# Kernel tuning notes

Measured on AMD Instinct MI355X. Metric: run time of the kernel, lower is better.

Reference implementation:

```python
import jax, jax.numpy as jnp
import numpy as np

B, S, I, H = 256, 50, 1024, 512
SENT, DOC = 512, 1024
SEGMENTS, MAXPOS = 4, 25
POS_SZ, SEG_SZ = 50, 50


def _gru_dir(xg, W_hh, b_hh):
    # xg: [S,B,3H] precomputed input gates; returns hidden states [S,B,H]
    Hh = W_hh.shape[1]

    def step(h, xg_t):
        hg = h @ W_hh.T + b_hh  # [B,3H]
        r = jax.nn.sigmoid(xg_t[:, :Hh] + hg[:, :Hh])
        z = jax.nn.sigmoid(xg_t[:, Hh:2 * Hh] + hg[:, Hh:2 * Hh])
        n = jnp.tanh(xg_t[:, 2 * Hh:] + r * hg[:, 2 * Hh:])
        h = (1.0 - z) * n + z * h
        return h, h

    h0 = jnp.zeros((xg.shape[1], Hh), xg.dtype)
    _, hs = jax.lax.scan(step, h0, xg)
    return hs


def setup_inputs() -> dict:
    key = jax.random.key(0)
    ks = jax.random.split(key, 24)
    sc = 0.05
    inp = {
        'x': jax.random.normal(ks[0], (B, S, I), jnp.float32),
        'num_sentences': jnp.full((B,), S, jnp.int32),
        # GRU forward direction
        'W_ih_f': jax.random.normal(ks[1], (3 * H, I), jnp.float32) * sc,
        'W_hh_f': jax.random.normal(ks[2], (3 * H, H), jnp.float32) * sc,
        'b_ih_f': jax.random.normal(ks[3], (3 * H,), jnp.float32) * sc,
        'b_hh_f': jax.random.normal(ks[4], (3 * H,), jnp.float32) * sc,
        # GRU backward direction
        'W_ih_b': jax.random.normal(ks[5], (3 * H, I), jnp.float32) * sc,
        'W_hh_b': jax.random.normal(ks[6], (3 * H, H), jnp.float32) * sc,
        'b_ih_b': jax.random.normal(ks[7], (3 * H,), jnp.float32) * sc,
        'b_hh_b': jax.random.normal(ks[8], (3 * H,), jnp.float32) * sc,
        # sentence_rep: Linear(2H -> SENT) + ReLU
        'W_sent': jax.random.normal(ks[9], (SENT, 2 * H), jnp.float32) * sc,
        'b_sent': jax.random.normal(ks[10], (SENT,), jnp.float32) * sc,
        # content_logits: Linear(SENT -> 1)
        'w_content': jax.random.normal(ks[11], (SENT,), jnp.float32) * sc,
        'b_content': jax.random.normal(ks[12], (1,), jnp.float32) * sc,
        # document_rep: Linear(SENT->DOC), tanh, Linear(DOC->SENT)
        'W_d1': jax.random.normal(ks[13], (DOC, SENT), jnp.float32) * sc,
        'b_d1': jax.random.normal(ks[14], (DOC,), jnp.float32) * sc,
        'W_d2': jax.random.normal(ks[15], (SENT, DOC), jnp.float32) * sc,
        'b_d2': jax.random.normal(ks[16], (SENT,), jnp.float32) * sc,
        # Bilinear(SENT, SENT, 1, bias=False) weight
        'W_sim': jax.random.normal(ks[17], (SENT, SENT), jnp.float32) * sc,
        'bias': jnp.zeros((1,), jnp.float32),
        # position / segment encoders (embedding row 0 is padding -> zeros)
        'pos_emb': (jax.random.normal(ks[18], (MAXPOS + 1, POS_SZ), jnp.float32) * sc).at[0].set(0.0),
        'pos_lin': jax.random.normal(ks[19], (POS_SZ,), jnp.float32) * sc,
        'seg_emb': (jax.random.normal(ks[20], (SEGMENTS + 1, SEG_SZ), jnp.float32) * sc).at[0].set(0.0),
        'seg_lin': jax.random.normal(ks[21], (SEG_SZ,), jnp.float32) * sc,
    }
    return inp


def reference(x, num_sentences, W_ih_f, W_hh_f, b_ih_f, b_hh_f,
              W_ih_b, W_hh_b, b_ih_b, b_hh_b,
              W_sent, b_sent, w_content, b_content,
              W_d1, b_d1, W_d2, b_d2, W_sim, bias,
              pos_emb, pos_lin, seg_emb, seg_lin):
    xs = jnp.transpose(x, (1, 0, 2))  # [S,B,I] (time-major, uniform lengths)

    # Bidirectional GRU
    xg_f = jnp.einsum('sbi,gi->sbg', xs, W_ih_f) + b_ih_f
    hs_f = _gru_dir(xg_f, W_hh_f, b_hh_f)  # [S,B,H]
    xg_b = jnp.einsum('sbi,gi->sbg', xs[::-1], W_ih_b) + b_ih_b
    hs_b = _gru_dir(xg_b, W_hh_b, b_hh_b)[::-1]  # [S,B,H]
    rnn_out = jnp.concatenate([hs_f, hs_b], axis=-1)  # [S,B,2H]
    rnn_out = jnp.transpose(rnn_out, (1, 0, 2))  # [B,S,2H]

    # sentence representations
    sent = jax.nn.relu(jnp.einsum('bsh,dh->bsd', rnn_out, W_sent) + b_sent)  # [B,S,SENT]

    content = jnp.einsum('bsd,d->bs', sent, w_content) + b_content[0]

    avg = sent.sum(axis=1) / num_sentences[:, None].astype(sent.dtype)  # [B,SENT]
    doc = jnp.tanh(avg @ W_d1.T + b_d1) @ W_d2.T + b_d2  # [B,SENT]
    salience = jnp.einsum('bsd,bd->bs', sent, doc)

    # position / segment logits (faithful to original ordering: rel computed pre-clamp)
    abs_pos = jnp.arange(1, S + 1)[None, :].astype(jnp.float32)  # [1,S]
    chunk = jnp.round(num_sentences.astype(jnp.float32) / SEGMENTS)[:, None]  # [B,1]
    rel = jnp.clip(jnp.ceil(abs_pos / chunk), 0, SEGMENTS).astype(jnp.int32)  # [B,S]
    abs_idx = jnp.clip(jnp.arange(1, S + 1), 0, MAXPOS)  # [S]
    pos_logits = pos_emb[abs_idx] @ pos_lin  # [S]
    seg_logits = seg_emb[rel] @ seg_lin  # [B,S]

    static = content + salience + pos_logits[None, :] + seg_logits + bias[0]  # [B,S]

    # sequential novelty scan
    def step(summary, inputs):
        s_t, static_t = inputs  # [B,SENT], [B]
        sim = jnp.einsum('bi,ij,bj->b', s_t, W_sim, jnp.tanh(summary))
        logit = static_t - sim
        summary = summary + s_t * jax.nn.sigmoid(logit)[:, None]
        return summary, logit

    sent_tm = jnp.transpose(sent, (1, 0, 2))  # [S,B,SENT]
    summary0 = jnp.zeros((x.shape[0], SENT), sent.dtype)
    _, logits = jax.lax.scan(step, summary0, (sent_tm, static.T))  # [S,B]
    return logits[:, :, None]  # [S,B,1]
```

## Files before the change

kernel.cpp:

```cpp
#include <hip/hip_runtime.h>
#include <hip/hip_bf16.h>
#include <math.h>

#define B_    256
#define S_    50
#define I_    1024
#define H_    512
#define G3_   1536
#define SENT_ 512
#define DOC_  1024

typedef short bf16x8 __attribute__((ext_vector_type(8)));
typedef float f32x4 __attribute__((ext_vector_type(4)));

__device__ __forceinline__ float sigf(float x) { return 1.0f / (1.0f + __expf(-x)); }

__device__ __forceinline__ void gload16(const void* g, void* l) {
  __builtin_amdgcn_global_load_lds((const __attribute__((address_space(1))) void*)g,
                                   (__attribute__((address_space(3))) void*)l, 16, 0, 0);
}

__global__ __launch_bounds__(256) void mfma_xg(
    const __hip_bfloat16* __restrict__ x,
    const __hip_bfloat16* __restrict__ Wf, const float* __restrict__ bf_,
    const __hip_bfloat16* __restrict__ Wb, const float* __restrict__ bb_,
    __hip_bfloat16* __restrict__ xgf, __hip_bfloat16* __restrict__ xgb) {
  __shared__ __align__(16) short As[128 * 64];
  __shared__ __align__(16) short Ws[128 * 64];
  const int dir = blockIdx.z;
  const __hip_bfloat16* W = dir ? Wb : Wf;
  const float* bias = dir ? bb_ : bf_;
  __hip_bfloat16* out = dir ? xgb : xgf;
  const int tid = threadIdx.x;
  const int m0 = blockIdx.y * 128, n0 = blockIdx.x * 128;
  const int s = blockIdx.y >> 1, b_base = (blockIdx.y & 1) * 128;
  const int s_eff = dir ? (S_ - 1 - s) : s;
  const int lane = tid & 63, w = tid >> 6;
  const int moff = (w & 1) * 64, noff = (w >> 1) * 64;
  const int frow = lane & 15, quad = lane >> 4;
  const int rr = tid >> 3, gs = tid & 7;
  f32x4 acc[4][4] = {};
  for (int kc = 0; kc < I_; kc += 64) {
#pragma unroll
    for (int iss = 0; iss < 4; iss++) {
      int r = iss * 32 + rr;
      int col = kc + ((gs ^ (r & 7)) << 3);
      gload16(x + ((size_t)(b_base + r) * S_ + s_eff) * I_ + col, &As[(iss * 256 + w * 64) * 8]);
    }
#pragma unroll
    for (int iss = 0; iss < 4; iss++) {
      int r = iss * 32 + rr;
      int col = kc + ((gs ^ (r & 7)) << 3);
      gload16(W + (size_t)(n0 + r) * I_ + col, &Ws[(iss * 256 + w * 64) * 8]);
    }
    __syncthreads();
#pragma unroll
    for (int ks = 0; ks < 2; ks++) {
      int kg = ks * 4 + quad;
      bf16x8 af[4], bfr[4];
#pragma unroll
      for (int mf = 0; mf < 4; mf++) {
        int r = moff + mf * 16 + frow;
        af[mf] = *(const bf16x8*)&As[(r * 8 + (kg ^ (r & 7))) * 8];
      }
#pragma unroll
      for (int nf = 0; nf < 4; nf++) {
        int r = noff + nf * 16 + frow;
        bfr[nf] = *(const bf16x8*)&Ws[(r * 8 + (kg ^ (r & 7))) * 8];
      }
#pragma unroll
      for (int mf = 0; mf < 4; mf++)
#pragma unroll
        for (int nf = 0; nf < 4; nf++)
          acc[mf][nf] = __builtin_amdgcn_mfma_f32_16x16x32_bf16(af[mf], bfr[nf], acc[mf][nf], 0, 0, 0);
    }
    __syncthreads();
  }
#pragma unroll
  for (int mf = 0; mf < 4; mf++) {
    int rowb = m0 + moff + mf * 16 + quad * 4;
#pragma unroll
    for (int nf = 0; nf < 4; nf++) {
      int col = n0 + noff + nf * 16 + frow;
      float bv = bias[col];
      f32x4 c = acc[mf][nf];
#pragma unroll
      for (int rg = 0; rg < 4; rg++)
        out[(size_t)(rowb + rg) * G3_ + col] = __float2bfloat16(c[rg] + bv);
    }
  }
}

template <int ACT, bool HASBIAS>
__global__ __launch_bounds__(256) void mfma_nt(
    const __hip_bfloat16* __restrict__ A, const __hip_bfloat16* __restrict__ W,
    const float* __restrict__ bias, __hip_bfloat16* __restrict__ outb, int N, int K) {
  __shared__ __align__(16) short As[128 * 64];
  __shared__ __align__(16) short Ws[128 * 64];
  const int tid = threadIdx.x;
  const int m0 = blockIdx.y * 128, n0 = blockIdx.x * 128;
  const int lane = tid & 63, w = tid >> 6;
  const int moff = (w & 1) * 64, noff = (w >> 1) * 64;
  const int frow = lane & 15, quad = lane >> 4;
  const int rr = tid >> 3, gs = tid & 7;
  f32x4 acc[4][4] = {};
  for (int kc = 0; kc < K; kc += 64) {
#pragma unroll
    for (int iss = 0; iss < 4; iss++) {
      int r = iss * 32 + rr;
      int col = kc + ((gs ^ (r & 7)) << 3);
      gload16(A + (size_t)(m0 + r) * K + col, &As[(iss * 256 + w * 64) * 8]);
    }
#pragma unroll
    for (int iss = 0; iss < 4; iss++) {
      int r = iss * 32 + rr;
      int col = kc + ((gs ^ (r & 7)) << 3);
      gload16(W + (size_t)(n0 + r) * K + col, &Ws[(iss * 256 + w * 64) * 8]);
    }
    __syncthreads();
#pragma unroll
    for (int ks = 0; ks < 2; ks++) {
      int kg = ks * 4 + quad;
      bf16x8 af[4], bfr[4];
#pragma unroll
      for (int mf = 0; mf < 4; mf++) {
        int r = moff + mf * 16 + frow;
        af[mf] = *(const bf16x8*)&As[(r * 8 + (kg ^ (r & 7))) * 8];
      }
#pragma unroll
      for (int nf = 0; nf < 4; nf++) {
        int r = noff + nf * 16 + frow;
        bfr[nf] = *(const bf16x8*)&Ws[(r * 8 + (kg ^ (r & 7))) * 8];
      }
#pragma unroll
      for (int mf = 0; mf < 4; mf++)
#pragma unroll
        for (int nf = 0; nf < 4; nf++)
          acc[mf][nf] = __builtin_amdgcn_mfma_f32_16x16x32_bf16(af[mf], bfr[nf], acc[mf][nf], 0, 0, 0);
    }
    __syncthreads();
  }
#pragma unroll
  for (int mf = 0; mf < 4; mf++) {
    int rowb = m0 + moff + mf * 16 + quad * 4;
#pragma unroll
    for (int nf = 0; nf < 4; nf++) {
      int col = n0 + noff + nf * 16 + frow;
      float bv = HASBIAS ? bias[col] : 0.f;
      f32x4 c = acc[mf][nf];
#pragma unroll
      for (int rg = 0; rg < 4; rg++) {
        float v = c[rg] + bv;
        if (ACT == 1) v = fmaxf(v, 0.f);
        outb[(size_t)(rowb + rg) * N + col] = __float2bfloat16(v);
      }
    }
  }
}

__global__ __launch_bounds__(256, 1) void gru_persistent(
    const __hip_bfloat16* __restrict__ xgf, const __hip_bfloat16* __restrict__ xgb,
    const __hip_bfloat16* __restrict__ Wpf, const __hip_bfloat16* __restrict__ Wpb,
    const float* __restrict__ bhhf, const float* __restrict__ bhhb,
    __hip_bfloat16* __restrict__ h16a, __hip_bfloat16* __restrict__ h16b,
    __hip_bfloat16* __restrict__ rnn,
    unsigned int* __restrict__ arrive) {
  const int bid = blockIdx.x;
  const int dir = bid >> 7;
  const int bt = (bid >> 5) & 3;
  const int jt = bid & 31;
  const int g8 = bid >> 5;
  const int tid = threadIdx.x;
  const int w = tid >> 6, lane = tid & 63;
  const int frow = lane & 15, quad = lane >> 4;
  const __hip_bfloat16* xg = dir ? xgb : xgf;
  const __hip_bfloat16* Wp = dir ? Wpb : Wpf;
  const float* bhh = dir ? bhhb : bhhf;

  unsigned int* my_flag = arrive + bid * 64;

  const int j = jt * 16 + frow;
  const int brow0 = bt * 64 + w * 16 + quad * 4;
  const float br = bhh[j], bz = bhh[H_ + j], bn = bhh[2 * H_ + j];

  bf16x8 wf[3][16];
#pragma unroll
  for (int g = 0; g < 3; g++)
#pragma unroll
    for (int ks = 0; ks < 16; ks++)
      wf[g][ks] = *(const bf16x8*)(Wp + (size_t)(jt * 48 + g * 16 + frow) * H_ + ks * 32 + quad * 8);

  float hreg[4] = {0.f, 0.f, 0.f, 0.f};
  union U16 { unsigned long long q[2]; bf16x8 v; };

  for (int t = 0; t < S_; t++) {
    const __hip_bfloat16* hp = (t & 1) ? h16b : h16a;
    __hip_bfloat16* hn = (t & 1) ? h16a : h16b;
    float xgv[4][3];
#pragma unroll
    for (int rg = 0; rg < 4; rg++) {
      const __hip_bfloat16* xr = xg + ((size_t)t * B_ + brow0 + rg) * G3_;
      xgv[rg][0] = __bfloat162float(xr[j]);
      xgv[rg][1] = __bfloat162float(xr[H_ + j]);
      xgv[rg][2] = __bfloat162float(xr[2 * H_ + j]);
    }
    const __hip_bfloat16* hprow = hp + (size_t)(dir * B_ + bt * 64 + w * 16 + frow) * H_;
    bf16x8 af[16];
#pragma unroll
    for (int ks = 0; ks < 16; ks++) {
      const unsigned long long* p = (const unsigned long long*)(hprow + ks * 32 + quad * 8);
      U16 u;
      u.q[0] = __hip_atomic_load(p, __ATOMIC_RELAXED, __HIP_MEMORY_SCOPE_AGENT);
      u.q[1] = __hip_atomic_load(p + 1, __ATOMIC_RELAXED, __HIP_MEMORY_SCOPE_AGENT);
      af[ks] = u.v;
    }
    f32x4 acc[3] = {};
#pragma unroll
    for (int ks = 0; ks < 16; ks++)
#pragma unroll
      for (int g = 0; g < 3; g++)
        acc[g] = __builtin_amdgcn_mfma_f32_16x16x32_bf16(af[ks], wf[g][ks], acc[g], 0, 0, 0);

    const int s_orig = dir ? (S_ - 1 - t) : t;
#pragma unroll
    for (int rg = 0; rg < 4; rg++) {
      int b = brow0 + rg;
      float r = sigf(xgv[rg][0] + acc[0][rg] + br);
      float z = sigf(xgv[rg][1] + acc[1][rg] + bz);
      float n = tanhf(xgv[rg][2] + r * (acc[2][rg] + bn));
      float h = (1.f - z) * n + z * hreg[rg];
      hreg[rg] = h;
      __hip_bfloat16 hb = __float2bfloat16(h);
      unsigned short us;
      __builtin_memcpy(&us, &hb, 2);
      __hip_atomic_store((unsigned short*)(hn + (size_t)(dir * B_ + b) * H_ + j), us,
                         __ATOMIC_RELAXED, __HIP_MEMORY_SCOPE_AGENT);
      rnn[((size_t)b * S_ + s_orig) * (2 * H_) + dir * H_ + j] = hb;
    }

    if (t + 1 < S_) {
      __syncthreads();
      if (tid == 0)
        __hip_atomic_store(my_flag, (unsigned)(t + 1), __ATOMIC_RELAXED,
                           __HIP_MEMORY_SCOPE_AGENT);
      if (w == 0) {
        unsigned int* fl = arrive + ((size_t)(g8 * 32 + (lane & 31))) * 64;
        for (int spin = 0; spin < (1 << 17); spin++) {
          unsigned v = (lane < 32)
                           ? __hip_atomic_load(fl, __ATOMIC_RELAXED, __HIP_MEMORY_SCOPE_AGENT)
                           : (unsigned)(t + 1);
          if (__ballot(v >= (unsigned)(t + 1)) == ~0ull) break;
          __builtin_amdgcn_s_sleep(1);
        }
      }
      __syncthreads();
    }
  }
}

template <int ACT>
__global__ __launch_bounds__(256) void gemm_nt(const float* __restrict__ A,
                                               const float* __restrict__ W,
                                               const float* __restrict__ bias,
                                               float* __restrict__ C, int N, int K) {
  __shared__ float As[16][68];
  __shared__ float Bs[16][68];
  const int t = threadIdx.x;
  const int tx = t & 15, ty = t >> 4;
  const int m0 = blockIdx.y * 64, n0 = blockIdx.x * 64;
  const int lr = t >> 2, lc = t & 3;
  const float* Arow = A + (size_t)(m0 + lr) * K;
  const float* Wrow = W + (size_t)(n0 + lr) * K;
  float acc[4][4] = {};
  for (int kc = 0; kc < K; kc += 16) {
    float4 av = *(const float4*)(Arow + kc + lc * 4);
    float4 wv = *(const float4*)(Wrow + kc + lc * 4);
    As[lc * 4 + 0][lr] = av.x; As[lc * 4 + 1][lr] = av.y;
    As[lc * 4 + 2][lr] = av.z; As[lc * 4 + 3][lr] = av.w;
    Bs[lc * 4 + 0][lr] = wv.x; Bs[lc * 4 + 1][lr] = wv.y;
    Bs[lc * 4 + 2][lr] = wv.z; Bs[lc * 4 + 3][lr] = wv.w;
    __syncthreads();
#pragma unroll
    for (int k = 0; k < 16; k++) {
      float4 a4 = *(const float4*)&As[k][ty * 4];
      float4 b4 = *(const float4*)&Bs[k][tx * 4];
      float ar[4] = {a4.x, a4.y, a4.z, a4.w};
      float br[4] = {b4.x, b4.y, b4.z, b4.w};
#pragma unroll
      for (int i = 0; i < 4; i++)
#pragma unroll
        for (int jx = 0; jx < 4; jx++) acc[i][jx] = fmaf(ar[i], br[jx], acc[i][jx]);
    }
    __syncthreads();
  }
  float4 bv = *(const float4*)&bias[n0 + tx * 4];
  float bb[4] = {bv.x, bv.y, bv.z, bv.w};
#pragma unroll
  for (int i = 0; i < 4; i++) {
    float o[4];
#pragma unroll
    for (int jx = 0; jx < 4; jx++) {
      float v = acc[i][jx] + bb[jx];
      if (ACT == 1) v = fmaxf(v, 0.f);
      if (ACT == 2) v = tanhf(v);
      o[jx] = v;
    }
    *(float4*)&C[(size_t)(m0 + ty * 4 + i) * N + n0 + tx * 4] = float4{o[0], o[1], o[2], o[3]};
  }
}

__global__ void cast_kernel(const float* __restrict__ in, __hip_bfloat16* __restrict__ out, int n) {
  int i = (blockIdx.x * blockDim.x + threadIdx.x) * 4;
  if (i + 3 < n) {
    float4 v = *(const float4*)(in + i);
    out[i + 0] = __float2bfloat16(v.x);
    out[i + 1] = __float2bfloat16(v.y);
    out[i + 2] = __float2bfloat16(v.z);
    out[i + 3] = __float2bfloat16(v.w);
  }
}

__global__ void pack_whh(const float* __restrict__ Whh, __hip_bfloat16* __restrict__ outp) {
  int idx = blockIdx.x * 256 + threadIdx.x;
  if (idx >= G3_ * H_) return;
  int k = idx & 511;
  int row = idx >> 9;
  int g = row >> 9, j = row & 511;
  int p = (j >> 4) * 48 + g * 16 + (j & 15);
  outp[(size_t)p * H_ + k] = __float2bfloat16(Whh[idx]);
}

__global__ void tcast_wsim(const float* __restrict__ Wsim, __hip_bfloat16* __restrict__ outT) {
  int idx = blockIdx.x * 256 + threadIdx.x;
  if (idx >= SENT_ * SENT_) return;
  int i = idx >> 9, j = idx & 511;
  outT[(size_t)j * SENT_ + i] = __float2bfloat16(Wsim[idx]);
}

__global__ __launch_bounds__(256) void avg_kernel(const __hip_bfloat16* __restrict__ sent,
                                                  const int* __restrict__ ns,
                                                  float* __restrict__ avg) {
  int b = blockIdx.x, tid = threadIdx.x;
  const __hip_bfloat16* base = sent + (size_t)b * S_ * SENT_;
  float a0 = 0.f, a1 = 0.f;
  for (int s = 0; s < S_; s++) {
    a0 += __bfloat162float(base[s * SENT_ + tid]);
    a1 += __bfloat162float(base[s * SENT_ + 256 + tid]);
  }
  float inv = 1.0f / (float)ns[b];
  avg[(size_t)b * SENT_ + tid] = a0 * inv;
  avg[(size_t)b * SENT_ + 256 + tid] = a1 * inv;
}

__global__ void posseg_kernel(const float* __restrict__ pos_emb, const float* __restrict__ pos_lin,
                              const float* __restrict__ seg_emb, const float* __restrict__ seg_lin,
                              float* __restrict__ pos_logits, float* __restrict__ seg_vals) {
  int tid = threadIdx.x;
  if (tid < S_) {
    int idx = tid + 1; if (idx > 25) idx = 25;
    float a = 0.f;
    for (int k = 0; k < 50; k++) a += pos_emb[idx * 50 + k] * pos_lin[k];
    pos_logits[tid] = a;
  }
  if (tid < 5) {
    float a = 0.f;
    for (int k = 0; k < 50; k++) a += seg_emb[tid * 50 + k] * seg_lin[k];
    seg_vals[tid] = a;
  }
}

__global__ __launch_bounds__(64) void static_kernel(
    const __hip_bfloat16* __restrict__ sent, const float* __restrict__ doc,
    const float* __restrict__ wcont, const float* __restrict__ bcont,
    const int* __restrict__ ns, const float* __restrict__ pos_logits,
    const float* __restrict__ seg_vals, const float* __restrict__ bias,
    float* __restrict__ st) {
  int bs = blockIdx.x;
  int b = bs / S_, s = bs % S_;
  int lane = threadIdx.x;
  const __hip_bfloat16* sr = sent + (size_t)bs * SENT_;
  const float* dr = doc + (size_t)b * SENT_;
  float a0 = 0.f, a1 = 0.f;
#pragma unroll
  for (int ii = 0; ii < 8; ii++) {
    int k = ii * 64 + lane;
    float v = __bfloat162float(sr[k]);
    a0 += v * wcont[k];
    a1 += v * dr[k];
  }
#pragma unroll
  for (int off = 32; off; off >>= 1) {
    a0 += __shfl_down(a0, off);
    a1 += __shfl_down(a1, off);
  }
  if (lane == 0) {
    float chunk = rintf((float)ns[b] * 0.25f);
    float relf = ceilf((float)(s + 1) / chunk);
    relf = fminf(fmaxf(relf, 0.f), 4.f);
    int rel = (int)relf;
    st[s * B_ + b] = a0 + bcont[0] + a1 + pos_logits[s] + seg_vals[rel] + bias[0];
  }
}

__global__ __launch_bounds__(256) void novelty_all(
    const __hip_bfloat16* __restrict__ sent, const __hip_bfloat16* __restrict__ U,
    const float* __restrict__ st, float* __restrict__ out) {
  __shared__ float wred[4];
  int b = blockIdx.x, tid = threadIdx.x;
  float s0 = 0.f, s1 = 0.f;
  for (int t = 0; t < S_; t++) {
    const __hip_bfloat16* ur = U + ((size_t)b * S_ + t) * SENT_;
    float p = __bfloat162float(ur[tid]) * tanhf(s0) +
              __bfloat162float(ur[tid + 256]) * tanhf(s1);
#pragma unroll
    for (int off = 32; off; off >>= 1) p += __shfl_down(p, off);
    if ((tid & 63) == 0) wred[tid >> 6] = p;
    __syncthreads();
    float sim = wred[0] + wred[1] + wred[2] + wred[3];
    float logit = st[t * B_ + b] - sim;
    if (tid == 0) out[(size_t)t * B_ + b] = logit;
    float sg = sigf(logit);
    const __hip_bfloat16* sr = sent + ((size_t)b * S_ + t) * SENT_;
    s0 += __bfloat162float(sr[tid]) * sg;
    s1 += __bfloat162float(sr[tid + 256]) * sg;
    __syncthreads();
  }
}

extern "C" void kernel_launch(void* const* d_in, const int* in_sizes, int n_in,
                              void* d_out, int out_size, void* d_ws, size_t ws_size,
                              hipStream_t stream) {
  const float* x = (const float*)d_in[0];
  const int* ns = (const int*)d_in[1];
  const float* Wihf = (const float*)d_in[2];
  const float* Whhf = (const float*)d_in[3];
  const float* bihf = (const float*)d_in[4];
  const float* bhhf = (const float*)d_in[5];
  const float* Wihb = (const float*)d_in[6];
  const float* Whhb = (const float*)d_in[7];
  const float* bihb = (const float*)d_in[8];
  const float* bhhb = (const float*)d_in[9];
  const float* Wsent = (const float*)d_in[10];
  const float* bsent = (const float*)d_in[11];
  const float* wcont = (const float*)d_in[12];
  const float* bcont = (const float*)d_in[13];
  const float* Wd1 = (const float*)d_in[14];
  const float* bd1 = (const float*)d_in[15];
  const float* Wd2 = (const float*)d_in[16];
  const float* bd2 = (const float*)d_in[17];
  const float* Wsim = (const float*)d_in[18];
  const float* bias = (const float*)d_in[19];
  const float* pos_emb = (const float*)d_in[20];
  const float* pos_lin = (const float*)d_in[21];
  const float* seg_emb = (const float*)d_in[22];
  const float* seg_lin = (const float*)d_in[23];
  float* out = (float*)d_out;

  char* base = (char*)d_ws;
  size_t off = 0;
  auto alloc = [&](size_t bytes) { char* p = base + off; off += (bytes + 255) & ~255ull; return p; };
  __hip_bfloat16* xgf_b  = (__hip_bfloat16*)alloc((size_t)S_ * B_ * G3_ * 2);
  __hip_bfloat16* xgb_b  = (__hip_bfloat16*)alloc((size_t)S_ * B_ * G3_ * 2);
  char* region1          = alloc((size_t)B_ * S_ * I_ * 2);
  __hip_bfloat16* x_bf   = (__hip_bfloat16*)region1;
  __hip_bfloat16* sent_b = (__hip_bfloat16*)region1;
  __hip_bfloat16* U_b    = (__hip_bfloat16*)(region1 + (size_t)B_ * S_ * SENT_ * 2);
  __hip_bfloat16* rnn_b  = (__hip_bfloat16*)alloc((size_t)B_ * S_ * 2 * H_ * 2);
  __hip_bfloat16* Wihf_b = (__hip_bfloat16*)alloc((size_t)G3_ * I_ * 2);
  __hip_bfloat16* Wihb_b = (__hip_bfloat16*)alloc((size_t)G3_ * I_ * 2);
  __hip_bfloat16* Wpf    = (__hip_bfloat16*)alloc((size_t)G3_ * H_ * 2);
  __hip_bfloat16* Wpb    = (__hip_bfloat16*)alloc((size_t)G3_ * H_ * 2);
  __hip_bfloat16* Wsent_b= (__hip_bfloat16*)alloc((size_t)SENT_ * 2 * H_ * 2);
  __hip_bfloat16* WsimT_b= (__hip_bfloat16*)alloc((size_t)SENT_ * SENT_ * 2);
  __hip_bfloat16* h16a   = (__hip_bfloat16*)alloc(2 * (size_t)B_ * H_ * 2);
  __hip_bfloat16* h16b   = (__hip_bfloat16*)alloc(2 * (size_t)B_ * H_ * 2);
  unsigned int* arrive   = (unsigned int*)alloc(256 * 64 * 4);
  float* avg             = (float*)alloc((size_t)B_ * SENT_ * 4);
  float* d1buf           = (float*)alloc((size_t)B_ * DOC_ * 4);
  float* doc             = (float*)alloc((size_t)B_ * SENT_ * 4);
  float* st              = (float*)alloc((size_t)S_ * B_ * 4);
  float* poslog          = (float*)alloc(256);
  float* segvals         = (float*)alloc(64);
  (void)ws_size;

  (void)hipMemsetAsync(h16a, 0, 2 * (size_t)B_ * H_ * 2, stream);
  (void)hipMemsetAsync(arrive, 0, 256 * 64 * 4, stream);

  cast_kernel<<<(B_ * S_ * I_ / 4 + 255) / 256, 256, 0, stream>>>(x, x_bf, B_ * S_ * I_);
  cast_kernel<<<(G3_ * I_ / 4 + 255) / 256, 256, 0, stream>>>(Wihf, Wihf_b, G3_ * I_);
  cast_kernel<<<(G3_ * I_ / 4 + 255) / 256, 256, 0, stream>>>(Wihb, Wihb_b, G3_ * I_);
  cast_kernel<<<(SENT_ * 2 * H_ / 4 + 255) / 256, 256, 0, stream>>>(Wsent, Wsent_b, SENT_ * 2 * H_);
  pack_whh<<<(G3_ * H_ + 255) / 256, 256, 0, stream>>>(Whhf, Wpf);
  pack_whh<<<(G3_ * H_ + 255) / 256, 256, 0, stream>>>(Whhb, Wpb);
  tcast_wsim<<<(SENT_ * SENT_ + 255) / 256, 256, 0, stream>>>(Wsim, WsimT_b);
  posseg_kernel<<<1, 64, 0, stream>>>(pos_emb, pos_lin, seg_emb, seg_lin, poslog, segvals);

  mfma_xg<<<dim3(G3_ / 128, (S_ * B_) / 128, 2), 256, 0, stream>>>(x_bf, Wihf_b, bihf, Wihb_b, bihb, xgf_b, xgb_b);

  gru_persistent<<<dim3(256), dim3(256), 0, stream>>>(
      xgf_b, xgb_b, Wpf, Wpb, bhhf, bhhb, h16a, h16b, rnn_b, arrive);

  mfma_nt<1, true><<<dim3(SENT_ / 128, (B_ * S_) / 128), 256, 0, stream>>>(rnn_b, Wsent_b, bsent, sent_b, SENT_, 2 * H_);
  avg_kernel<<<B_, 256, 0, stream>>>(sent_b, ns, avg);
  gemm_nt<2><<<dim3(DOC_ / 64, B_ / 64), 256, 0, stream>>>(avg, Wd1, bd1, d1buf, DOC_, SENT_);
  gemm_nt<0><<<dim3(SENT_ / 64, B_ / 64), 256, 0, stream>>>(d1buf, Wd2, bd2, doc, SENT_, DOC_);
  static_kernel<<<B_ * S_, 64, 0, stream>>>(sent_b, doc, wcont, bcont, ns, poslog, segvals, bias, st);

  mfma_nt<0, false><<<dim3(SENT_ / 128, (B_ * S_) / 128), 256, 0, stream>>>(sent_b, WsimT_b, nullptr, U_b, SENT_, SENT_);

  novelty_all<<<B_, 256, 0, stream>>>(sent_b, U_b, st, out);
}
```

Before: 779.8 us.

## Retile persistent GRU into 16-block groups with LDS-shared hidden state; fuse prep kernels

```diff
diff --git a/kernel.cpp b/kernel.cpp
--- a/kernel.cpp
+++ b/kernel.cpp
@@ -165,22 +165,25 @@
     __hip_bfloat16* __restrict__ h16a, __hip_bfloat16* __restrict__ h16b,
     __hip_bfloat16* __restrict__ rnn,
     unsigned int* __restrict__ arrive) {
+  __shared__ __align__(16) short Hs[32 * 512];
   const int bid = blockIdx.x;
   const int dir = bid >> 7;
-  const int bt = (bid >> 5) & 3;
-  const int jt = bid & 31;
-  const int g8 = bid >> 5;
+  const int bt = (bid >> 4) & 7;
+  const int jt = bid & 15;
+  const int gi = bid >> 4;
   const int tid = threadIdx.x;
   const int w = tid >> 6, lane = tid & 63;
   const int frow = lane & 15, quad = lane >> 4;
+  const int wm = w & 1, wn = w >> 1;
   const __hip_bfloat16* xg = dir ? xgb : xgf;
   const __hip_bfloat16* Wp = dir ? Wpb : Wpf;
   const float* bhh = dir ? bhhb : bhhf;
 
-  unsigned int* my_flag = arrive + bid * 64;
-
-  const int j = jt * 16 + frow;
-  const int brow0 = bt * 64 + w * 16 + quad * 4;
+  unsigned int* my_flag = arrive + (size_t)bid * 64;
+
+  const int j = jt * 32 + wn * 16 + frow;
+  const int brow0 = bt * 32 + wm * 16 + quad * 4;
+  const int ar = wm * 16 + frow;
   const float br = bhh[j], bz = bhh[H_ + j], bn = bhh[2 * H_ + j];
 
   bf16x8 wf[3][16];
@@ -188,7 +191,8 @@
   for (int g = 0; g < 3; g++)
 #pragma unroll
     for (int ks = 0; ks < 16; ks++)
-      wf[g][ks] = *(const bf16x8*)(Wp + (size_t)(jt * 48 + g * 16 + frow) * H_ + ks * 32 + quad * 8);
+      wf[g][ks] = *(const bf16x8*)(Wp + (size_t)((jt * 2 + wn) * 48 + g * 16 + frow) * H_ +
+                                   ks * 32 + quad * 8);
 
   float hreg[4] = {0.f, 0.f, 0.f, 0.f};
   union U16 { unsigned long long q[2]; bf16x8 v; };
@@ -204,15 +208,25 @@
       xgv[rg][1] = __bfloat162float(xr[H_ + j]);
       xgv[rg][2] = __bfloat162float(xr[2 * H_ + j]);
     }
-    const __hip_bfloat16* hprow = hp + (size_t)(dir * B_ + bt * 64 + w * 16 + frow) * H_;
-    bf16x8 af[16];
-#pragma unroll
-    for (int ks = 0; ks < 16; ks++) {
-      const unsigned long long* p = (const unsigned long long*)(hprow + ks * 32 + quad * 8);
+    const __hip_bfloat16* hbase = hp + (size_t)(dir * B_ + bt * 32) * H_;
+#pragma unroll
+    for (int i = 0; i < 8; i++) {
+      int c = i * 256 + tid;
+      int r = c >> 6, kg = c & 63;
+      const unsigned long long* p = (const unsigned long long*)(hbase + (size_t)r * H_ + kg * 8);
       U16 u;
       u.q[0] = __hip_atomic_load(p, __ATOMIC_RELAXED, __HIP_MEMORY_SCOPE_AGENT);
       u.q[1] = __hip_atomic_load(p + 1, __ATOMIC_RELAXED, __HIP_MEMORY_SCOPE_AGENT);
-      af[ks] = u.v;
+      int q = r * 64 + (kg & 56) + ((kg & 7) ^ (r & 7));
+      *(bf16x8*)&Hs[q * 8] = u.v;
+    }
+    __syncthreads();
+    bf16x8 af[16];
+#pragma unroll
+    for (int ks = 0; ks < 16; ks++) {
+      int g2 = ks * 4 + quad;
+      int q = ar * 64 + (g2 & 56) + ((g2 & 7) ^ (ar & 7));
+      af[ks] = *(const bf16x8*)&Hs[q * 8];
     }
     f32x4 acc[3] = {};
 #pragma unroll
@@ -244,9 +258,9 @@
         __hip_atomic_store(my_flag, (unsigned)(t + 1), __ATOMIC_RELAXED,
                            __HIP_MEMORY_SCOPE_AGENT);
       if (w == 0) {
-        unsigned int* fl = arrive + ((size_t)(g8 * 32 + (lane & 31))) * 64;
+        unsigned int* fl = arrive + (size_t)(gi * 16 + (lane & 15)) * 64;
         for (int spin = 0; spin < (1 << 17); spin++) {
-          unsigned v = (lane < 32)
+          unsigned v = (lane < 16)
                            ? __hip_atomic_load(fl, __ATOMIC_RELAXED, __HIP_MEMORY_SCOPE_AGENT)
                            : (unsigned)(t + 1);
           if (__ballot(v >= (unsigned)(t + 1)) == ~0ull) break;
@@ -309,6 +323,79 @@
   }
 }
 
+#define PREP_CAST1   1536
+#define PREP_CAST2   3072
+#define PREP_CAST3   3584
+#define PREP_PACK1   4352
+#define PREP_PACK2   5120
+#define PREP_TSIM    6144
+#define PREP_ZH      6272
+#define PREP_ZF      6288
+#define PREP_POS     6289
+__global__ __launch_bounds__(256) void prep_all(
+    const float* __restrict__ Wihf, const float* __restrict__ Wihb,
+    const float* __restrict__ Wsent, const float* __restrict__ Whhf,
+    const float* __restrict__ Whhb, const float* __restrict__ Wsim,
+    const float* __restrict__ pos_emb, const float* __restrict__ pos_lin,
+    const float* __restrict__ seg_emb, const float* __restrict__ seg_lin,
+    __hip_bfloat16* __restrict__ Wihf_b, __hip_bfloat16* __restrict__ Wihb_b,
+    __hip_bfloat16* __restrict__ Wsent_b, __hip_bfloat16* __restrict__ Wpf,
+    __hip_bfloat16* __restrict__ Wpb, __hip_bfloat16* __restrict__ WsimT_b,
+    __hip_bfloat16* __restrict__ h16a, unsigned int* __restrict__ arrive,
+    float* __restrict__ pos_logits, float* __restrict__ seg_vals) {
+  const int blk = blockIdx.x, tid = threadIdx.x;
+  if (blk < PREP_CAST2) {
+    const float* src = (blk < PREP_CAST1) ? Wihf : Wihb;
+    __hip_bfloat16* dst = (blk < PREP_CAST1) ? Wihf_b : Wihb_b;
+    int lb = (blk < PREP_CAST1) ? blk : blk - PREP_CAST1;
+    int i = lb * 1024 + tid * 4;
+    float4 v = *(const float4*)(src + i);
+    dst[i] = __float2bfloat16(v.x); dst[i + 1] = __float2bfloat16(v.y);
+    dst[i + 2] = __float2bfloat16(v.z); dst[i + 3] = __float2bfloat16(v.w);
+  } else if (blk < PREP_CAST3) {
+    int i = (blk - PREP_CAST2) * 1024 + tid * 4;
+    float4 v = *(const float4*)(Wsent + i);
+    Wsent_b[i] = __float2bfloat16(v.x); Wsent_b[i + 1] = __float2bfloat16(v.y);
+    Wsent_b[i + 2] = __float2bfloat16(v.z); Wsent_b[i + 3] = __float2bfloat16(v.w);
+  } else if (blk < PREP_PACK2) {
+    const float* src = (blk < PREP_PACK1) ? Whhf : Whhb;
+    __hip_bfloat16* dst = (blk < PREP_PACK1) ? Wpf : Wpb;
+    int lb = (blk < PREP_PACK1) ? blk - PREP_CAST3 : blk - PREP_PACK1;
+    int e = lb * 1024 + tid * 4;
+    int row = e >> 9, k = e & 511;
+    int g = row >> 9, j = row & 511;
+    int p = (j >> 4) * 48 + g * 16 + (j & 15);
+    float4 v = *(const float4*)(src + (size_t)row * 512 + k);
+    __hip_bfloat16* d = dst + (size_t)p * 512 + k;
+    d[0] = __float2bfloat16(v.x); d[1] = __float2bfloat16(v.y);
+    d[2] = __float2bfloat16(v.z); d[3] = __float2bfloat16(v.w);
+  } else if (blk < PREP_TSIM) {
+    int idx = (blk - PREP_PACK2) * 256 + tid;
+    int i = idx >> 9, j = idx & 511;
+    WsimT_b[(size_t)j * 512 + i] = __float2bfloat16(Wsim[idx]);
+  } else if (blk < PREP_ZH) {
+    int i = (blk - PREP_TSIM) * 2048 + tid * 8;
+    float4 z = {0.f, 0.f, 0.f, 0.f};
+    *(float4*)((short*)h16a + i) = z;
+  } else if (blk < PREP_ZF) {
+    int i = (blk - PREP_ZH) * 1024 + tid * 4;
+    float4 z = {0.f, 0.f, 0.f, 0.f};
+    *(float4*)(arrive + i) = z;
+  } else {
+    if (tid < S_) {
+      int idx = tid + 1; if (idx > 25) idx = 25;
+      float a = 0.f;
+      for (int k = 0; k < 50; k++) a += pos_emb[idx * 50 + k] * pos_lin[k];
+      pos_logits[tid] = a;
+    }
+    if (tid < 5) {
+      float a = 0.f;
+      for (int k = 0; k < 50; k++) a += seg_emb[tid * 50 + k] * seg_lin[k];
+      seg_vals[tid] = a;
+    }
+  }
+}
+
 __global__ void cast_kernel(const float* __restrict__ in, __hip_bfloat16* __restrict__ out, int n) {
   int i = (blockIdx.x * blockDim.x + threadIdx.x) * 4;
   if (i + 3 < n) {
@@ -318,23 +405,6 @@
     out[i + 2] = __float2bfloat16(v.z);
     out[i + 3] = __float2bfloat16(v.w);
   }
-}
-
-__global__ void pack_whh(const float* __restrict__ Whh, __hip_bfloat16* __restrict__ outp) {
-  int idx = blockIdx.x * 256 + threadIdx.x;
-  if (idx >= G3_ * H_) return;
-  int k = idx & 511;
-  int row = idx >> 9;
-  int g = row >> 9, j = row & 511;
-  int p = (j >> 4) * 48 + g * 16 + (j & 15);
-  outp[(size_t)p * H_ + k] = __float2bfloat16(Whh[idx]);
-}
-
-__global__ void tcast_wsim(const float* __restrict__ Wsim, __hip_bfloat16* __restrict__ outT) {
-  int idx = blockIdx.x * 256 + threadIdx.x;
-  if (idx >= SENT_ * SENT_) return;
-  int i = idx >> 9, j = idx & 511;
-  outT[(size_t)j * SENT_ + i] = __float2bfloat16(Wsim[idx]);
 }
 
 __global__ __launch_bounds__(256) void avg_kernel(const __hip_bfloat16* __restrict__ sent,
@@ -350,23 +420,6 @@
   float inv = 1.0f / (float)ns[b];
   avg[(size_t)b * SENT_ + tid] = a0 * inv;
   avg[(size_t)b * SENT_ + 256 + tid] = a1 * inv;
-}
-
-__global__ void posseg_kernel(const float* __restrict__ pos_emb, const float* __restrict__ pos_lin,
-                              const float* __restrict__ seg_emb, const float* __restrict__ seg_lin,
-                              float* __restrict__ pos_logits, float* __restrict__ seg_vals) {
-  int tid = threadIdx.x;
-  if (tid < S_) {
-    int idx = tid + 1; if (idx > 25) idx = 25;
-    float a = 0.f;
-    for (int k = 0; k < 50; k++) a += pos_emb[idx * 50 + k] * pos_lin[k];
-    pos_logits[tid] = a;
-  }
-  if (tid < 5) {
-    float a = 0.f;
-    for (int k = 0; k < 50; k++) a += seg_emb[tid * 50 + k] * seg_lin[k];
-    seg_vals[tid] = a;
-  }
 }
 
 __global__ __launch_bounds__(64) void static_kernel(
@@ -483,17 +536,10 @@
   float* segvals         = (float*)alloc(64);
   (void)ws_size;
 
-  (void)hipMemsetAsync(h16a, 0, 2 * (size_t)B_ * H_ * 2, stream);
-  (void)hipMemsetAsync(arrive, 0, 256 * 64 * 4, stream);
-
+  prep_all<<<PREP_POS + 1, 256, 0, stream>>>(
+      Wihf, Wihb, Wsent, Whhf, Whhb, Wsim, pos_emb, pos_lin, seg_emb, seg_lin,
+      Wihf_b, Wihb_b, Wsent_b, Wpf, Wpb, WsimT_b, h16a, arrive, poslog, segvals);
   cast_kernel<<<(B_ * S_ * I_ / 4 + 255) / 256, 256, 0, stream>>>(x, x_bf, B_ * S_ * I_);
-  cast_kernel<<<(G3_ * I_ / 4 + 255) / 256, 256, 0, stream>>>(Wihf, Wihf_b, G3_ * I_);
-  cast_kernel<<<(G3_ * I_ / 4 + 255) / 256, 256, 0, stream>>>(Wihb, Wihb_b, G3_ * I_);
-  cast_kernel<<<(SENT_ * 2 * H_ / 4 + 255) / 256, 256, 0, stream>>>(Wsent, Wsent_b, SENT_ * 2 * H_);
-  pack_whh<<<(G3_ * H_ + 255) / 256, 256, 0, stream>>>(Whhf, Wpf);
-  pack_whh<<<(G3_ * H_ + 255) / 256, 256, 0, stream>>>(Whhb, Wpb);
-  tcast_wsim<<<(SENT_ * SENT_ + 255) / 256, 256, 0, stream>>>(Wsim, WsimT_b);
-  posseg_kernel<<<1, 64, 0, stream>>>(pos_emb, pos_lin, seg_emb, seg_lin, poslog, segvals);
 
   mfma_xg<<<dim3(G3_ / 128, (S_ * B_) / 128, 2), 256, 0, stream>>>(x_bf, Wihf_b, bihf, Wihb_b, bihb, xgf_b, xgb_b);
 
```

New measurement: 695.5 us. 1.12x faster.
